# Performance work log

Hardware: AMD Instinct MI355X
Metric: run time of the kernel (lower is better)

## Reference

```python
import jax, jax.numpy as jnp
import numpy as np

N_NODES = 100000
N_EDGES = 600000
N_FEAT = 128
N_HID = 128
N_GRAPHS = 256


def gcn_conv(x, src, dst, W, b, n_nodes):
    # PyG GCNConv: h = x @ W; add self-loops; sym-normalize; scatter-add; + bias
    h = x @ W  # [N, H]
    loop = jnp.arange(n_nodes)
    s = jnp.concatenate([src, loop])
    d = jnp.concatenate([dst, loop])
    deg = jax.ops.segment_sum(jnp.ones_like(d, dtype=h.dtype), d, num_segments=n_nodes)
    dinv = jnp.where(deg > 0, jax.lax.rsqrt(deg), 0.0)
    norm = dinv[s] * dinv[d]  # [E+N]
    msg = h[s] * norm[:, None]  # gather + scale
    out = jax.ops.segment_sum(msg, d, num_segments=n_nodes)  # scatter-add
    return out + b


def setup_inputs() -> dict:
    key = jax.random.key(0)
    ks = jax.random.split(key, 12)
    x = jax.random.normal(ks[0], (N_NODES, N_FEAT), dtype=jnp.float32)
    edge_index = jax.random.randint(ks[1], (2, N_EDGES), 0, N_NODES, dtype=jnp.int64)
    batch = jnp.sort(jax.random.randint(ks[2], (N_NODES,), 0, N_GRAPHS, dtype=jnp.int64))
    def lin(k, fi, fo):
        s = 1.0 / np.sqrt(fi)
        return jax.random.uniform(k, (fi, fo), jnp.float32, -s, s)
    params = {
        'W1': lin(ks[3], N_FEAT, N_HID), 'b1': jnp.zeros((N_HID,), jnp.float32),
        'W2': lin(ks[4], N_HID, N_HID), 'b2': jnp.zeros((N_HID,), jnp.float32),
        'W3': lin(ks[5], N_HID, N_HID), 'b3': jnp.zeros((N_HID,), jnp.float32),
        'W4': lin(ks[6], N_HID, N_HID), 'b4': jnp.zeros((N_HID,), jnp.float32),
        'Ws1': lin(ks[7], N_HID, N_HID), 'bs1': jnp.zeros((N_HID,), jnp.float32),
        'Ws2': lin(ks[8], N_HID, 1), 'bs2': jnp.zeros((1,), jnp.float32),
    }
    return {'x': x, 'edge_index': edge_index, 'batch': batch, **params}


def reference(x, edge_index, batch, W1, b1, W2, b2, W3, b3, W4, b4, Ws1, bs1, Ws2, bs2):
    src, dst = edge_index[0], edge_index[1]
    h = x
    # 2 conv blocks = 4 GCNConv layers, each followed by ReLU
    for W, b in ((W1, b1), (W2, b2), (W3, b3), (W4, b4)):
        h = jax.nn.relu(gcn_conv(h, src, dst, W, b, N_NODES))
    # global mean pool over nodes per graph
    sums = jax.ops.segment_sum(h, batch, num_segments=N_GRAPHS)  # [G, H]
    cnt = jax.ops.segment_sum(jnp.ones((h.shape[0],), h.dtype), batch, num_segments=N_GRAPHS)
    pooled = sums / jnp.maximum(cnt, 1.0)[:, None]
    # summary MLP: Linear -> ReLU -> Linear(->1)
    out = jax.nn.relu(pooled @ Ws1 + bs1) @ Ws2 + bs2  # [G, 1]
    return out
```

## Files before the change

### kernel.cpp

```cpp
#include <hip/hip_runtime.h>

#define N_NODES 100000
#define N_EDGES 600000
#define NF 128
#define NG 256

typedef _Float16 f16;
typedef f16 half8 __attribute__((ext_vector_type(8)));
typedef f16 half4v __attribute__((ext_vector_type(4)));
typedef float float4v __attribute__((ext_vector_type(4)));


__global__ void k_count(const int* __restrict__ ei, int* __restrict__ counts) {
    int e = blockIdx.x * 256 + threadIdx.x;
    if (e < N_EDGES) atomicAdd(&counts[ei[N_EDGES + e]], 1);
}

__global__ void k_scan1(const int* __restrict__ counts, int* __restrict__ row_ptr,
                        int* __restrict__ bsums, float* __restrict__ dinv) {
    __shared__ int s[256];
    int b = blockIdx.x, t = threadIdx.x;
    int base = b * 2048 + t * 8;
    int local[8];
    int sum = 0;
#pragma unroll
    for (int q = 0; q < 8; q++) {
        int idx = base + q;
        int v = (idx < N_NODES) ? counts[idx] : 0;
        if (idx < N_NODES) dinv[idx] = 1.0f / sqrtf((float)(v + 1));
        local[q] = sum;
        sum += v;
    }
    s[t] = sum;
    __syncthreads();
    for (int off = 1; off < 256; off <<= 1) {
        int v = 0;
        if (t >= off) v = s[t - off];
        __syncthreads();
        s[t] += v;
        __syncthreads();
    }
    int excl = s[t] - sum;
#pragma unroll
    for (int q = 0; q < 8; q++) {
        int idx = base + q;
        if (idx < N_NODES) row_ptr[idx] = excl + local[q];
    }
    if (t == 255) bsums[b] = s[255];
}

__global__ void k_scan2(int* bsums, int nb) {
    if (threadIdx.x == 0 && blockIdx.x == 0) {
        int run = 0;
        for (int b = 0; b < nb; b++) { int v = bsums[b]; bsums[b] = run; run += v; }
    }
}

__global__ void k_scan3(int* __restrict__ row_ptr, const int* __restrict__ bsums,
                        int* __restrict__ cursor) {
    int i = blockIdx.x * 256 + threadIdx.x;
    if (i < N_NODES) {
        int v = row_ptr[i] + bsums[i >> 11];
        row_ptr[i] = v;
        cursor[i] = v;
        if (i == 0) row_ptr[N_NODES] = N_EDGES;
    }
}

__global__ void k_fill(const int* __restrict__ ei, int* __restrict__ cursor,
                       int* __restrict__ col) {
    int e = blockIdx.x * 256 + threadIdx.x;
    if (e < N_EDGES) {
        int d = ei[N_EDGES + e];
        int p = atomicAdd(&cursor[d], 1);
        col[p] = ei[e];
    }
}


__global__ void k_wprep(const float* __restrict__ W1, const float* __restrict__ W2,
                        const float* __restrict__ W3, const float* __restrict__ W4,
                        f16* __restrict__ wtH, f16* __restrict__ wtL) {
    int idx = blockIdx.x * 256 + threadIdx.x;
    int layer = idx >> 14;
    int rem = idx & 16383;
    int n = rem >> 7, k = rem & 127;
    const float* W = (layer == 0) ? W1 : (layer == 1) ? W2 : (layer == 2) ? W3 : W4;
    float w = W[k * NF + n];
    f16 h = (f16)w;
    f16 l = (f16)(w - (float)h);
    wtH[layer * 16384 + n * NF + k] = h;
    wtL[layer * 16384 + n * NF + k] = l;
}


template <int XIN>
__global__ __launch_bounds__(256) void k_gemm_mfma(
    const float* __restrict__ X, const f16* __restrict__ A,
    const f16* __restrict__ WTH, const f16* __restrict__ WTL,
    f16* __restrict__ Z, int M) {
    __shared__ __align__(16) f16 As[64 * 136];

    const int t = threadIdx.x;
    const int row0 = blockIdx.x * 64;
    const int wave = t >> 6;
    const int lane = t & 63;
    const int nl = lane & 15;
    const int quad = lane >> 4;

    half8 fbh[4][2], fbl[4][2];
#pragma unroll
    for (int s = 0; s < 4; s++)
#pragma unroll
        for (int ct = 0; ct < 2; ct++) {
            int ng = wave * 32 + ct * 16 + nl;
            size_t wo = (size_t)ng * NF + s * 32 + quad * 8;
            fbh[s][ct] = *(const half8*)(WTH + wo);
            fbl[s][ct] = *(const half8*)(WTL + wo);
        }

    if (XIN) {
#pragma unroll
        for (int q = 0; q < 8; q++) {
            int lin = t + q * 256;
            int r = lin >> 5, c4 = lin & 31;
            float4 v = make_float4(0.f, 0.f, 0.f, 0.f);
            if (row0 + r < M) v = ((const float4*)(X + (size_t)(row0 + r) * NF))[c4];
            half4v hv = {(f16)v.x, (f16)v.y, (f16)v.z, (f16)v.w};
            *(half4v*)&As[r * 136 + c4 * 4] = hv;
        }
    } else {
#pragma unroll
        for (int q = 0; q < 4; q++) {
            int lin = t + q * 256;
            int r = lin >> 4, c8 = lin & 15;
            half8 v = {};
            if (row0 + r < M) v = *(const half8*)(A + (size_t)(row0 + r) * NF + c8 * 8);
            *(half8*)&As[r * 136 + c8 * 8] = v;
        }
    }
    __syncthreads();

    float4v acc[2][4];
#pragma unroll
    for (int ct = 0; ct < 2; ct++)
#pragma unroll
        for (int rt = 0; rt < 4; rt++) acc[ct][rt] = (float4v)0.f;

#pragma unroll
    for (int s = 0; s < 4; s++) {
        half8 fa[4];
#pragma unroll
        for (int rt = 0; rt < 4; rt++)
            fa[rt] = *(half8*)&As[(rt * 16 + nl) * 136 + s * 32 + quad * 8];
#pragma unroll
        for (int ct = 0; ct < 2; ct++)
#pragma unroll
            for (int rt = 0; rt < 4; rt++) {
                acc[ct][rt] = __builtin_amdgcn_mfma_f32_16x16x32_f16(fa[rt], fbh[s][ct], acc[ct][rt], 0, 0, 0);
                acc[ct][rt] = __builtin_amdgcn_mfma_f32_16x16x32_f16(fa[rt], fbl[s][ct], acc[ct][rt], 0, 0, 0);
            }
    }

    __syncthreads();
#pragma unroll
    for (int ct = 0; ct < 2; ct++)
#pragma unroll
        for (int rt = 0; rt < 4; rt++)
#pragma unroll
            for (int r = 0; r < 4; r++)
                As[(rt * 16 + quad * 4 + r) * 136 + wave * 32 + ct * 16 + nl] =
                    (f16)acc[ct][rt][r];
    __syncthreads();
#pragma unroll
    for (int q = 0; q < 4; q++) {
        int lin = t + q * 256;
        int r = lin >> 4, c8 = lin & 15;
        if (row0 + r < M)
            *(half8*)(Z + (size_t)(row0 + r) * NF + c8 * 8) = *(half8*)&As[r * 136 + c8 * 8];
    }
}


#define ACHUNK 4

__global__ __launch_bounds__(256) void k_agg(const f16* __restrict__ z,
                                             const float* __restrict__ dinv,
                                             const int* __restrict__ row_ptr,
                                             const int* __restrict__ col,
                                             const float* __restrict__ bias,
                                             f16* __restrict__ h) {
    const int t = threadIdx.x;
    const int slot = t >> 4;
    const int fl = t & 15;
    const int sbase = (t & 48);
    const int n0 = (blockIdx.x * 16 + slot) * ACHUNK;
    const half8* z8 = (const half8*)z;

    float bb[8];
    {
        float4 b0 = ((const float4*)bias)[fl * 2];
        float4 b1 = ((const float4*)bias)[fl * 2 + 1];
        bb[0] = b0.x; bb[1] = b0.y; bb[2] = b0.z; bb[3] = b0.w;
        bb[4] = b1.x; bb[5] = b1.y; bb[6] = b1.z; bb[7] = b1.w;
    }

    for (int n = n0; n < n0 + ACHUNK && n < N_NODES; n++) {
        const float di = dinv[n];
        const int beg = row_ptr[n];
        const int end = row_ptr[n + 1];

        float acc[8];
        {
            half8 v = z8[(size_t)n * 16 + fl];
            float w = di * di;
#pragma unroll
            for (int j = 0; j < 8; j++) acc[j] = bb[j] + (float)v[j] * w;
        }

        for (int c = beg; c < end; c += 16) {
            int mcnt = end - c; if (mcnt > 16) mcnt = 16;
            int ce = c + fl;
            int colv = (ce < end) ? col[ce] : 0;
            float dv = dinv[colv];

            int j = 0;
            for (; j + 1 < mcnt; j += 2) {
                int s1 = __shfl(colv, sbase + j, 64);
                float w1 = __shfl(dv, sbase + j, 64) * di;
                int s2 = __shfl(colv, sbase + j + 1, 64);
                float w2 = __shfl(dv, sbase + j + 1, 64) * di;
                half8 v1 = z8[(size_t)s1 * 16 + fl];
                half8 v2 = z8[(size_t)s2 * 16 + fl];
#pragma unroll
                for (int q = 0; q < 8; q++) acc[q] += (float)v1[q] * w1;
#pragma unroll
                for (int q = 0; q < 8; q++) acc[q] += (float)v2[q] * w2;
            }
            if (j < mcnt) {
                int s1 = __shfl(colv, sbase + j, 64);
                float w1 = __shfl(dv, sbase + j, 64) * di;
                half8 v1 = z8[(size_t)s1 * 16 + fl];
#pragma unroll
                for (int q = 0; q < 8; q++) acc[q] += (float)v1[q] * w1;
            }
        }

        half8 o;
#pragma unroll
        for (int j = 0; j < 8; j++) o[j] = (f16)fmaxf(acc[j], 0.f);
        ((half8*)h)[(size_t)n * 16 + fl] = o;
    }
}


#define POOL_CHUNK 64

__global__ __launch_bounds__(128) void k_pool2(const f16* __restrict__ h,
                                               const int* __restrict__ batch,
                                               float* __restrict__ pooled) {
    int f = threadIdx.x;
    int n0 = blockIdx.x * POOL_CHUNK;
    int n1 = n0 + POOL_CHUNK;
    if (n1 > N_NODES) n1 = N_NODES;
    if (n0 >= N_NODES) return;
    int g = batch[n0];
    float acc = 0.f;
    for (int n = n0; n < n1; n++) {
        int gn = batch[n];
        if (gn != g) {
            atomicAdd(&pooled[g * NF + f], acc);
            acc = 0.f;
            g = gn;
        }
        acc += (float)h[(size_t)n * NF + f];
    }
    atomicAdd(&pooled[g * NF + f], acc);
}


__global__ void k_mlp(const float* __restrict__ pooled, const int* __restrict__ batch,
                      const float* __restrict__ Ws1, const float* __restrict__ bs1,
                      const float* __restrict__ Ws2, const float* __restrict__ bs2,
                      float* __restrict__ out) {
    __shared__ float row[NF];
    __shared__ float red[NF];
    int g = blockIdx.x, f = threadIdx.x;
    int lo = 0, hi = N_NODES;
    while (lo < hi) { int mid = (lo + hi) >> 1; if (batch[mid] < g) lo = mid + 1; else hi = mid; }
    int start = lo;
    hi = N_NODES;
    while (lo < hi) { int mid = (lo + hi) >> 1; if (batch[mid] < g + 1) lo = mid + 1; else hi = mid; }
    float cnt = (float)(lo - start);
    row[f] = pooled[g * NF + f] / fmaxf(cnt, 1.f);
    __syncthreads();
    float t = bs1[f];
    for (int k = 0; k < NF; k++) t += row[k] * Ws1[k * NF + f];
    t = fmaxf(t, 0.f);
    red[f] = t * Ws2[f];
    __syncthreads();
    for (int s = 64; s > 0; s >>= 1) {
        if (f < s) red[f] += red[f + s];
        __syncthreads();
    }
    if (f == 0) out[g] = red[0] + bs2[0];
}


extern "C" void kernel_launch(void* const* d_in, const int* in_sizes, int n_in,
                              void* d_out, int out_size, void* d_ws, size_t ws_size,
                              hipStream_t stream) {
    const float* x    = (const float*)d_in[0];
    const int*   ei   = (const int*)d_in[1];
    const int*   batch= (const int*)d_in[2];
    const float* W1 = (const float*)d_in[3];  const float* b1 = (const float*)d_in[4];
    const float* W2 = (const float*)d_in[5];  const float* b2 = (const float*)d_in[6];
    const float* W3 = (const float*)d_in[7];  const float* b3 = (const float*)d_in[8];
    const float* W4 = (const float*)d_in[9];  const float* b4 = (const float*)d_in[10];
    const float* Ws1= (const float*)d_in[11]; const float* bs1= (const float*)d_in[12];
    const float* Ws2= (const float*)d_in[13]; const float* bs2= (const float*)d_in[14];
    float* out = (float*)d_out;

    char* ws = (char*)d_ws;
    size_t off = 0;
    auto alloc = [&](size_t bytes) {
        void* p = ws + off;
        off += (bytes + 255) & ~(size_t)255;
        return p;
    };
    f16*   bufZ   = (f16*)alloc((size_t)N_NODES * NF * 2);
    f16*   bufH   = (f16*)alloc((size_t)N_NODES * NF * 2);
    f16*   wtH    = (f16*)alloc((size_t)4 * NF * NF * 2);
    f16*   wtL    = (f16*)alloc((size_t)4 * NF * NF * 2);
    int*   counts = (int*)alloc((size_t)N_NODES * 4);
    int*   row_ptr= (int*)alloc((size_t)(N_NODES + 1) * 4);
    int*   cursor = (int*)alloc((size_t)N_NODES * 4);
    int*   col    = (int*)alloc((size_t)N_EDGES * 4);
    int*   bsums  = (int*)alloc(64 * 4);
    float* dinv   = (float*)alloc((size_t)N_NODES * 4);
    float* pooled = (float*)alloc((size_t)NG * NF * 4);

    hipMemsetAsync(counts, 0, (size_t)N_NODES * 4, stream);
    hipMemsetAsync(pooled, 0, (size_t)NG * NF * 4, stream);
    k_count<<<(N_EDGES + 255) / 256, 256, 0, stream>>>(ei, counts);
    int nscan = (N_NODES + 2047) / 2048;
    k_scan1<<<nscan, 256, 0, stream>>>(counts, row_ptr, bsums, dinv);
    k_scan2<<<1, 64, 0, stream>>>(bsums, nscan);
    k_scan3<<<(N_NODES + 255) / 256, 256, 0, stream>>>(row_ptr, bsums, cursor);
    k_fill<<<(N_EDGES + 255) / 256, 256, 0, stream>>>(ei, cursor, col);
    k_wprep<<<256, 256, 0, stream>>>(W1, W2, W3, W4, wtH, wtL);

    int gblocks = (N_NODES + 63) / 64;
    int ablocks = (N_NODES + 16 * ACHUNK - 1) / (16 * ACHUNK);
    k_gemm_mfma<1><<<gblocks, 256, 0, stream>>>(x, nullptr, wtH, wtL, bufZ, N_NODES);
    k_agg<<<ablocks, 256, 0, stream>>>(bufZ, dinv, row_ptr, col, b1, bufH);
    k_gemm_mfma<0><<<gblocks, 256, 0, stream>>>(nullptr, bufH, wtH + 16384, wtL + 16384, bufZ, N_NODES);
    k_agg<<<ablocks, 256, 0, stream>>>(bufZ, dinv, row_ptr, col, b2, bufH);
    k_gemm_mfma<0><<<gblocks, 256, 0, stream>>>(nullptr, bufH, wtH + 32768, wtL + 32768, bufZ, N_NODES);
    k_agg<<<ablocks, 256, 0, stream>>>(bufZ, dinv, row_ptr, col, b3, bufH);
    k_gemm_mfma<0><<<gblocks, 256, 0, stream>>>(nullptr, bufH, wtH + 49152, wtL + 49152, bufZ, N_NODES);
    k_agg<<<ablocks, 256, 0, stream>>>(bufZ, dinv, row_ptr, col, b4, bufH);

    int pblocks = (N_NODES + POOL_CHUNK - 1) / POOL_CHUNK;
    k_pool2<<<pblocks, 128, 0, stream>>>(bufH, batch, pooled);
    k_mlp<<<NG, 128, 0, stream>>>(pooled, batch, Ws1, bs1, Ws2, bs2, out);
}
```

Measured before the change: 427.9 us.

## Fuse aggregation with next-layer GEMM and fold pooling into last aggregation

Each GCN aggregation now writes its ReLU output into shared memory, and the same block immediately runs the next layer's MFMA GEMM on that tile. This removes the round trip of the hidden activation buffer through global memory and three kernel launches. The final aggregation accumulates per-graph sums in registers and atomically adds them into the pooled buffer, which replaces the separate pool kernel. The cost is that the weight fragments are held in registers while the irregular gather runs, which may lower occupancy for the latency-bound aggregation.

```diff
diff --git a/kernel.cpp b/kernel.cpp
--- a/kernel.cpp
+++ b/kernel.cpp
@@ -94,9 +94,8 @@
 }
 
 
-template <int XIN>
-__global__ __launch_bounds__(256) void k_gemm_mfma(
-    const float* __restrict__ X, const f16* __restrict__ A,
+__global__ __launch_bounds__(256) void k_gemm_x(
+    const float* __restrict__ X,
     const f16* __restrict__ WTH, const f16* __restrict__ WTL,
     f16* __restrict__ Z, int M) {
     __shared__ __align__(16) f16 As[64 * 136];
@@ -119,25 +118,14 @@
             fbl[s][ct] = *(const half8*)(WTL + wo);
         }
 
-    if (XIN) {
-#pragma unroll
-        for (int q = 0; q < 8; q++) {
-            int lin = t + q * 256;
-            int r = lin >> 5, c4 = lin & 31;
-            float4 v = make_float4(0.f, 0.f, 0.f, 0.f);
-            if (row0 + r < M) v = ((const float4*)(X + (size_t)(row0 + r) * NF))[c4];
-            half4v hv = {(f16)v.x, (f16)v.y, (f16)v.z, (f16)v.w};
-            *(half4v*)&As[r * 136 + c4 * 4] = hv;
-        }
-    } else {
-#pragma unroll
-        for (int q = 0; q < 4; q++) {
-            int lin = t + q * 256;
-            int r = lin >> 4, c8 = lin & 15;
-            half8 v = {};
-            if (row0 + r < M) v = *(const half8*)(A + (size_t)(row0 + r) * NF + c8 * 8);
-            *(half8*)&As[r * 136 + c8 * 8] = v;
-        }
+#pragma unroll
+    for (int q = 0; q < 8; q++) {
+        int lin = t + q * 256;
+        int r = lin >> 5, c4 = lin & 31;
+        float4 v = make_float4(0.f, 0.f, 0.f, 0.f);
+        if (row0 + r < M) v = ((const float4*)(X + (size_t)(row0 + r) * NF))[c4];
+        half4v hv = {(f16)v.x, (f16)v.y, (f16)v.z, (f16)v.w};
+        *(half4v*)&As[r * 136 + c4 * 4] = hv;
     }
     __syncthreads();
 
@@ -182,14 +170,148 @@
 }
 
 
+__global__ __launch_bounds__(256) void k_fused(
+    const f16* __restrict__ z, const float* __restrict__ dinv,
+    const int* __restrict__ row_ptr, const int* __restrict__ col,
+    const float* __restrict__ bias,
+    const f16* __restrict__ WTH, const f16* __restrict__ WTL,
+    f16* __restrict__ Zout) {
+    __shared__ __align__(16) f16 As[64 * 136];
+
+    const int t = threadIdx.x;
+    const int row0 = blockIdx.x * 64;
+    const int wave = t >> 6;
+    const int lane = t & 63;
+    const int nl = lane & 15;
+    const int quad = lane >> 4;
+
+    half8 fbh[4][2], fbl[4][2];
+#pragma unroll
+    for (int s = 0; s < 4; s++)
+#pragma unroll
+        for (int ct = 0; ct < 2; ct++) {
+            int ng = wave * 32 + ct * 16 + nl;
+            size_t wo = (size_t)ng * NF + s * 32 + quad * 8;
+            fbh[s][ct] = *(const half8*)(WTH + wo);
+            fbl[s][ct] = *(const half8*)(WTL + wo);
+        }
+
+    {
+        const int slot = t >> 4;
+        const int fl = t & 15;
+        const int sbase = (t & 48);
+        const int n0 = row0 + slot * 4;
+        const half8* z8 = (const half8*)z;
+
+        float bb[8];
+        {
+            float4 b0 = ((const float4*)bias)[fl * 2];
+            float4 b1 = ((const float4*)bias)[fl * 2 + 1];
+            bb[0] = b0.x; bb[1] = b0.y; bb[2] = b0.z; bb[3] = b0.w;
+            bb[4] = b1.x; bb[5] = b1.y; bb[6] = b1.z; bb[7] = b1.w;
+        }
+
+#pragma unroll
+        for (int i = 0; i < 4; i++) {
+            int n = n0 + i;
+            int r = slot * 4 + i;
+            if (n >= N_NODES) {
+                *(half8*)&As[r * 136 + fl * 8] = (half8){};
+                continue;
+            }
+            const float di = dinv[n];
+            const int beg = row_ptr[n];
+            const int end = row_ptr[n + 1];
+
+            float acc[8];
+            {
+                half8 v = z8[(size_t)n * 16 + fl];
+                float w = di * di;
+#pragma unroll
+                for (int j = 0; j < 8; j++) acc[j] = bb[j] + (float)v[j] * w;
+            }
+            for (int c = beg; c < end; c += 16) {
+                int mcnt = end - c; if (mcnt > 16) mcnt = 16;
+                int ce = c + fl;
+                int colv = (ce < end) ? col[ce] : 0;
+                float dv = dinv[colv];
+                int j = 0;
+                for (; j + 1 < mcnt; j += 2) {
+                    int s1 = __shfl(colv, sbase + j, 64);
+                    float w1 = __shfl(dv, sbase + j, 64) * di;
+                    int s2 = __shfl(colv, sbase + j + 1, 64);
+                    float w2 = __shfl(dv, sbase + j + 1, 64) * di;
+                    half8 v1 = z8[(size_t)s1 * 16 + fl];
+                    half8 v2 = z8[(size_t)s2 * 16 + fl];
+#pragma unroll
+                    for (int q = 0; q < 8; q++) acc[q] += (float)v1[q] * w1;
+#pragma unroll
+                    for (int q = 0; q < 8; q++) acc[q] += (float)v2[q] * w2;
+                }
+                if (j < mcnt) {
+                    int s1 = __shfl(colv, sbase + j, 64);
+                    float w1 = __shfl(dv, sbase + j, 64) * di;
+                    half8 v1 = z8[(size_t)s1 * 16 + fl];
+#pragma unroll
+                    for (int q = 0; q < 8; q++) acc[q] += (float)v1[q] * w1;
+                }
+            }
+            half8 o;
+#pragma unroll
+            for (int j = 0; j < 8; j++) o[j] = (f16)fmaxf(acc[j], 0.f);
+            *(half8*)&As[r * 136 + fl * 8] = o;
+        }
+    }
+    __syncthreads();
+
+    float4v acc[2][4];
+#pragma unroll
+    for (int ct = 0; ct < 2; ct++)
+#pragma unroll
+        for (int rt = 0; rt < 4; rt++) acc[ct][rt] = (float4v)0.f;
+
+#pragma unroll
+    for (int s = 0; s < 4; s++) {
+        half8 fa[4];
+#pragma unroll
+        for (int rt = 0; rt < 4; rt++)
+            fa[rt] = *(half8*)&As[(rt * 16 + nl) * 136 + s * 32 + quad * 8];
+#pragma unroll
+        for (int ct = 0; ct < 2; ct++)
+#pragma unroll
+            for (int rt = 0; rt < 4; rt++) {
+                acc[ct][rt] = __builtin_amdgcn_mfma_f32_16x16x32_f16(fa[rt], fbh[s][ct], acc[ct][rt], 0, 0, 0);
+                acc[ct][rt] = __builtin_amdgcn_mfma_f32_16x16x32_f16(fa[rt], fbl[s][ct], acc[ct][rt], 0, 0, 0);
+            }
+    }
+
+    __syncthreads();
+#pragma unroll
+    for (int ct = 0; ct < 2; ct++)
+#pragma unroll
+        for (int rt = 0; rt < 4; rt++)
+#pragma unroll
+            for (int r = 0; r < 4; r++)
+                As[(rt * 16 + quad * 4 + r) * 136 + wave * 32 + ct * 16 + nl] =
+                    (f16)acc[ct][rt][r];
+    __syncthreads();
+#pragma unroll
+    for (int q = 0; q < 4; q++) {
+        int lin = t + q * 256;
+        int r = lin >> 4, c8 = lin & 15;
+        if (row0 + r < N_NODES)
+            *(half8*)(Zout + (size_t)(row0 + r) * NF + c8 * 8) = *(half8*)&As[r * 136 + c8 * 8];
+    }
+}
+
+
 #define ACHUNK 4
 
-__global__ __launch_bounds__(256) void k_agg(const f16* __restrict__ z,
-                                             const float* __restrict__ dinv,
-                                             const int* __restrict__ row_ptr,
-                                             const int* __restrict__ col,
-                                             const float* __restrict__ bias,
-                                             f16* __restrict__ h) {
+__global__ __launch_bounds__(256) void k_agg_pool(
+    const f16* __restrict__ z, const float* __restrict__ dinv,
+    const int* __restrict__ row_ptr, const int* __restrict__ col,
+    const float* __restrict__ bias, const int* __restrict__ batch,
+    float* __restrict__ pooled) {
     const int t = threadIdx.x;
     const int slot = t >> 4;
     const int fl = t & 15;
@@ -205,6 +327,11 @@
         bb[4] = b1.x; bb[5] = b1.y; bb[6] = b1.z; bb[7] = b1.w;
     }
 
+    int gcur = -1;
+    float ps[8];
+#pragma unroll
+    for (int j = 0; j < 8; j++) ps[j] = 0.f;
+
     for (int n = n0; n < n0 + ACHUNK && n < N_NODES; n++) {
         const float di = dinv[n];
         const int beg = row_ptr[n];
@@ -217,13 +344,11 @@
 #pragma unroll
             for (int j = 0; j < 8; j++) acc[j] = bb[j] + (float)v[j] * w;
         }
-
         for (int c = beg; c < end; c += 16) {
             int mcnt = end - c; if (mcnt > 16) mcnt = 16;
             int ce = c + fl;
             int colv = (ce < end) ? col[ce] : 0;
             float dv = dinv[colv];
-
             int j = 0;
             for (; j + 1 < mcnt; j += 2) {
                 int s1 = __shfl(colv, sbase + j, 64);
@@ -246,36 +371,25 @@
             }
         }
 
-        half8 o;
-#pragma unroll
-        for (int j = 0; j < 8; j++) o[j] = (f16)fmaxf(acc[j], 0.f);
-        ((half8*)h)[(size_t)n * 16 + fl] = o;
-    }
-}
-
-
-#define POOL_CHUNK 64
-
-__global__ __launch_bounds__(128) void k_pool2(const f16* __restrict__ h,
-                                               const int* __restrict__ batch,
-                                               float* __restrict__ pooled) {
-    int f = threadIdx.x;
-    int n0 = blockIdx.x * POOL_CHUNK;
-    int n1 = n0 + POOL_CHUNK;
-    if (n1 > N_NODES) n1 = N_NODES;
-    if (n0 >= N_NODES) return;
-    int g = batch[n0];
-    float acc = 0.f;
-    for (int n = n0; n < n1; n++) {
-        int gn = batch[n];
-        if (gn != g) {
-            atomicAdd(&pooled[g * NF + f], acc);
-            acc = 0.f;
-            g = gn;
-        }
-        acc += (float)h[(size_t)n * NF + f];
-    }
-    atomicAdd(&pooled[g * NF + f], acc);
+        int g = batch[n];
+        if (g != gcur) {
+            if (gcur >= 0) {
+#pragma unroll
+                for (int j = 0; j < 8; j++)
+                    atomicAdd(&pooled[gcur * NF + fl * 8 + j], ps[j]);
+            }
+            gcur = g;
+#pragma unroll
+            for (int j = 0; j < 8; j++) ps[j] = 0.f;
+        }
+#pragma unroll
+        for (int j = 0; j < 8; j++) ps[j] += (float)(f16)fmaxf(acc[j], 0.f);
+    }
+    if (gcur >= 0) {
+#pragma unroll
+        for (int j = 0; j < 8; j++)
+            atomicAdd(&pooled[gcur * NF + fl * 8 + j], ps[j]);
+    }
 }
 
 
@@ -329,7 +443,7 @@
         return p;
     };
     f16*   bufZ   = (f16*)alloc((size_t)N_NODES * NF * 2);
-    f16*   bufH   = (f16*)alloc((size_t)N_NODES * NF * 2);
+    f16*   bufZ2  = (f16*)alloc((size_t)N_NODES * NF * 2);
     f16*   wtH    = (f16*)alloc((size_t)4 * NF * NF * 2);
     f16*   wtL    = (f16*)alloc((size_t)4 * NF * NF * 2);
     int*   counts = (int*)alloc((size_t)N_NODES * 4);
@@ -351,17 +465,13 @@
     k_wprep<<<256, 256, 0, stream>>>(W1, W2, W3, W4, wtH, wtL);
 
     int gblocks = (N_NODES + 63) / 64;
-    int ablocks = (N_NODES + 16 * ACHUNK - 1) / (16 * ACHUNK);
-    k_gemm_mfma<1><<<gblocks, 256, 0, stream>>>(x, nullptr, wtH, wtL, bufZ, N_NODES);
-    k_agg<<<ablocks, 256, 0, stream>>>(bufZ, dinv, row_ptr, col, b1, bufH);
-    k_gemm_mfma<0><<<gblocks, 256, 0, stream>>>(nullptr, bufH, wtH + 16384, wtL + 16384, bufZ, N_NODES);
-    k_agg<<<ablocks, 256, 0, stream>>>(bufZ, dinv, row_ptr, col, b2, bufH);
-    k_gemm_mfma<0><<<gblocks, 256, 0, stream>>>(nullptr, bufH, wtH + 32768, wtL + 32768, bufZ, N_NODES);
-    k_agg<<<ablocks, 256, 0, stream>>>(bufZ, dinv, row_ptr, col, b3, bufH);
-    k_gemm_mfma<0><<<gblocks, 256, 0, stream>>>(nullptr, bufH, wtH + 49152, wtL + 49152, bufZ, N_NODES);
-    k_agg<<<ablocks, 256, 0, stream>>>(bufZ, dinv, row_ptr, col, b4, bufH);
-
-    int pblocks = (N_NODES + POOL_CHUNK - 1) / POOL_CHUNK;
-    k_pool2<<<pblocks, 128, 0, stream>>>(bufH, batch, pooled);
+    k_gemm_x<<<gblocks, 256, 0, stream>>>(x, wtH, wtL, bufZ, N_NODES);
+    k_fused<<<gblocks, 256, 0, stream>>>(bufZ, dinv, row_ptr, col, b1,
+                                         wtH + 16384, wtL + 16384, bufZ2);
+    k_fused<<<gblocks, 256, 0, stream>>>(bufZ2, dinv, row_ptr, col, b2,
+                                         wtH + 32768, wtL + 32768, bufZ);
+    k_fused<<<gblocks, 256, 0, stream>>>(bufZ, dinv, row_ptr, col, b3,
+                                         wtH + 49152, wtL + 49152, bufZ2);
+    k_agg_pool<<<gblocks, 256, 0, stream>>>(bufZ2, dinv, row_ptr, col, b4, batch, pooled);
     k_mlp<<<NG, 128, 0, stream>>>(pooled, batch, Ws1, bs1, Ws2, bs2, out);
 }
```

After: 535.2 us. 25.1% more time.

## Pack edge source and dinv into CSR entries and fuse preprocessing kernels

Applied to the files above, without the earlier changes.

Stores each CSR edge as an (src, dinv[src]) pair, so aggregation no longer does a dependent random gather into dinv per edge. The scan2 kernel is dropped by having each scan3 block sum the preceding block totals itself. Weight preparation is folded into the fill kernel, and the aggregation output uses nontemporal stores. Together these cut launch count and per-edge latency, at the cost of a larger edge array and redundant prefix sums in scan3.

```diff
diff --git a/kernel.cpp b/kernel.cpp
--- a/kernel.cpp
+++ b/kernel.cpp
@@ -49,18 +49,19 @@
     if (t == 255) bsums[b] = s[255];
 }
 
-__global__ void k_scan2(int* bsums, int nb) {
-    if (threadIdx.x == 0 && blockIdx.x == 0) {
-        int run = 0;
-        for (int b = 0; b < nb; b++) { int v = bsums[b]; bsums[b] = run; run += v; }
-    }
-}
-
 __global__ void k_scan3(int* __restrict__ row_ptr, const int* __restrict__ bsums,
                         int* __restrict__ cursor) {
+    __shared__ int pre;
+    if (threadIdx.x == 0) {
+        int g = blockIdx.x >> 3;
+        int s = 0;
+        for (int j = 0; j < g; j++) s += bsums[j];
+        pre = s;
+    }
+    __syncthreads();
     int i = blockIdx.x * 256 + threadIdx.x;
     if (i < N_NODES) {
-        int v = row_ptr[i] + bsums[i >> 11];
+        int v = row_ptr[i] + pre;
         row_ptr[i] = v;
         cursor[i] = v;
         if (i == 0) row_ptr[N_NODES] = N_EDGES;
@@ -68,29 +69,29 @@
 }
 
 __global__ void k_fill(const int* __restrict__ ei, int* __restrict__ cursor,
-                       int* __restrict__ col) {
+                       const float* __restrict__ dinv, int2* __restrict__ edge2,
+                       const float* __restrict__ W1, const float* __restrict__ W2,
+                       const float* __restrict__ W3, const float* __restrict__ W4,
+                       f16* __restrict__ wtH, f16* __restrict__ wtL) {
     int e = blockIdx.x * 256 + threadIdx.x;
     if (e < N_EDGES) {
+        int src = ei[e];
         int d = ei[N_EDGES + e];
         int p = atomicAdd(&cursor[d], 1);
-        col[p] = ei[e];
-    }
-}
-
-
-__global__ void k_wprep(const float* __restrict__ W1, const float* __restrict__ W2,
-                        const float* __restrict__ W3, const float* __restrict__ W4,
-                        f16* __restrict__ wtH, f16* __restrict__ wtL) {
-    int idx = blockIdx.x * 256 + threadIdx.x;
-    int layer = idx >> 14;
-    int rem = idx & 16383;
-    int n = rem >> 7, k = rem & 127;
-    const float* W = (layer == 0) ? W1 : (layer == 1) ? W2 : (layer == 2) ? W3 : W4;
-    float w = W[k * NF + n];
-    f16 h = (f16)w;
-    f16 l = (f16)(w - (float)h);
-    wtH[layer * 16384 + n * NF + k] = h;
-    wtL[layer * 16384 + n * NF + k] = l;
+        edge2[p] = make_int2(src, __float_as_int(dinv[src]));
+    }
+    if (blockIdx.x < 256) {
+        int idx = blockIdx.x * 256 + threadIdx.x;
+        int layer = idx >> 14;
+        int rem = idx & 16383;
+        int n = rem >> 7, k = rem & 127;
+        const float* W = (layer == 0) ? W1 : (layer == 1) ? W2 : (layer == 2) ? W3 : W4;
+        float w = W[k * NF + n];
+        f16 h = (f16)w;
+        f16 l = (f16)(w - (float)h);
+        wtH[layer * 16384 + n * NF + k] = h;
+        wtL[layer * 16384 + n * NF + k] = l;
+    }
 }
 
 
@@ -187,7 +188,7 @@
 __global__ __launch_bounds__(256) void k_agg(const f16* __restrict__ z,
                                              const float* __restrict__ dinv,
                                              const int* __restrict__ row_ptr,
-                                             const int* __restrict__ col,
+                                             const int2* __restrict__ edge2,
                                              const float* __restrict__ bias,
                                              f16* __restrict__ h) {
     const int t = threadIdx.x;
@@ -221,15 +222,16 @@
         for (int c = beg; c < end; c += 16) {
             int mcnt = end - c; if (mcnt > 16) mcnt = 16;
             int ce = c + fl;
-            int colv = (ce < end) ? col[ce] : 0;
-            float dv = dinv[colv];
+            int2 ev = (ce < end) ? edge2[ce] : make_int2(n, 0);
+            int colv = ev.x;
+            float wv = __int_as_float(ev.y);
 
             int j = 0;
             for (; j + 1 < mcnt; j += 2) {
                 int s1 = __shfl(colv, sbase + j, 64);
-                float w1 = __shfl(dv, sbase + j, 64) * di;
+                float w1 = __shfl(wv, sbase + j, 64) * di;
                 int s2 = __shfl(colv, sbase + j + 1, 64);
-                float w2 = __shfl(dv, sbase + j + 1, 64) * di;
+                float w2 = __shfl(wv, sbase + j + 1, 64) * di;
                 half8 v1 = z8[(size_t)s1 * 16 + fl];
                 half8 v2 = z8[(size_t)s2 * 16 + fl];
 #pragma unroll
@@ -239,7 +241,7 @@
             }
             if (j < mcnt) {
                 int s1 = __shfl(colv, sbase + j, 64);
-                float w1 = __shfl(dv, sbase + j, 64) * di;
+                float w1 = __shfl(wv, sbase + j, 64) * di;
                 half8 v1 = z8[(size_t)s1 * 16 + fl];
 #pragma unroll
                 for (int q = 0; q < 8; q++) acc[q] += (float)v1[q] * w1;
@@ -249,7 +251,7 @@
         half8 o;
 #pragma unroll
         for (int j = 0; j < 8; j++) o[j] = (f16)fmaxf(acc[j], 0.f);
-        ((half8*)h)[(size_t)n * 16 + fl] = o;
+        __builtin_nontemporal_store(o, (half8*)h + (size_t)n * 16 + fl);
     }
 }
 
@@ -335,7 +337,7 @@
     int*   counts = (int*)alloc((size_t)N_NODES * 4);
     int*   row_ptr= (int*)alloc((size_t)(N_NODES + 1) * 4);
     int*   cursor = (int*)alloc((size_t)N_NODES * 4);
-    int*   col    = (int*)alloc((size_t)N_EDGES * 4);
+    int2*  edge2  = (int2*)alloc((size_t)N_EDGES * 8);
     int*   bsums  = (int*)alloc(64 * 4);
     float* dinv   = (float*)alloc((size_t)N_NODES * 4);
     float* pooled = (float*)alloc((size_t)NG * NF * 4);
@@ -345,21 +347,20 @@
     k_count<<<(N_EDGES + 255) / 256, 256, 0, stream>>>(ei, counts);
     int nscan = (N_NODES + 2047) / 2048;
     k_scan1<<<nscan, 256, 0, stream>>>(counts, row_ptr, bsums, dinv);
-    k_scan2<<<1, 64, 0, stream>>>(bsums, nscan);
     k_scan3<<<(N_NODES + 255) / 256, 256, 0, stream>>>(row_ptr, bsums, cursor);
-    k_fill<<<(N_EDGES + 255) / 256, 256, 0, stream>>>(ei, cursor, col);
-    k_wprep<<<256, 256, 0, stream>>>(W1, W2, W3, W4, wtH, wtL);
+    k_fill<<<(N_EDGES + 255) / 256, 256, 0, stream>>>(ei, cursor, dinv, edge2,
+                                                      W1, W2, W3, W4, wtH, wtL);
 
     int gblocks = (N_NODES + 63) / 64;
     int ablocks = (N_NODES + 16 * ACHUNK - 1) / (16 * ACHUNK);
     k_gemm_mfma<1><<<gblocks, 256, 0, stream>>>(x, nullptr, wtH, wtL, bufZ, N_NODES);
-    k_agg<<<ablocks, 256, 0, stream>>>(bufZ, dinv, row_ptr, col, b1, bufH);
+    k_agg<<<ablocks, 256, 0, stream>>>(bufZ, dinv, row_ptr, edge2, b1, bufH);
     k_gemm_mfma<0><<<gblocks, 256, 0, stream>>>(nullptr, bufH, wtH + 16384, wtL + 16384, bufZ, N_NODES);
-    k_agg<<<ablocks, 256, 0, stream>>>(bufZ, dinv, row_ptr, col, b2, bufH);
+    k_agg<<<ablocks, 256, 0, stream>>>(bufZ, dinv, row_ptr, edge2, b2, bufH);
     k_gemm_mfma<0><<<gblocks, 256, 0, stream>>>(nullptr, bufH, wtH + 32768, wtL + 32768, bufZ, N_NODES);
-    k_agg<<<ablocks, 256, 0, stream>>>(bufZ, dinv, row_ptr, col, b3, bufH);
+    k_agg<<<ablocks, 256, 0, stream>>>(bufZ, dinv, row_ptr, edge2, b3, bufH);
     k_gemm_mfma<0><<<gblocks, 256, 0, stream>>>(nullptr, bufH, wtH + 49152, wtL + 49152, bufZ, N_NODES);
-    k_agg<<<ablocks, 256, 0, stream>>>(bufZ, dinv, row_ptr, col, b4, bufH);
+    k_agg<<<ablocks, 256, 0, stream>>>(bufZ, dinv, row_ptr, edge2, b4, bufH);
 
     int pblocks = (N_NODES + POOL_CHUNK - 1) / POOL_CHUNK;
     k_pool2<<<pblocks, 128, 0, stream>>>(bufH, batch, pooled);
```

Result: no change. 436.4 us (+2.0%).
